# Performance work log

Measured on AMD Instinct MI355X. Metric: run time of the kernel, lower is better.

The kernel has to match this reference:

```python
import jax, jax.numpy as jnp
import numpy as np

N, D, H = 4096, 1024, 16
GAMMA = 1.0


def setup_inputs() -> dict:
    key = jax.random.key(0)
    ks = jax.random.split(key, 10)
    s = 1.0 / np.sqrt(D)
    return {
        "x": jax.random.normal(ks[0], (N, D), jnp.float32),
        "h": jax.random.normal(ks[1], (N,), jnp.float32),
        "Wq": jax.random.normal(ks[2], (D, D), jnp.float32) * s,
        "bq": jax.random.normal(ks[3], (D,), jnp.float32) * s,
        "Wk": jax.random.normal(ks[4], (D, D), jnp.float32) * s,
        "bk": jax.random.normal(ks[5], (D,), jnp.float32) * s,
        "Wv": jax.random.normal(ks[6], (D, D), jnp.float32) * s,
        "bv": jax.random.normal(ks[7], (D,), jnp.float32) * s,
        "Wo": jax.random.normal(ks[8], (D, D), jnp.float32) * s,
        "bo": jax.random.normal(ks[9], (D,), jnp.float32) * s,
    }


def reference(x, h, Wq, bq, Wk, bk, Wv, bv, Wo, bo):
    n, d = x.shape
    d_head = d // H
    # torch Linear: y = x @ W.T + b
    q = (x @ Wq.T + bq).reshape(n, H, d_head)
    k = (x @ Wk.T + bk).reshape(n, H, d_head)
    v = (x @ Wv.T + bv).reshape(n, H, d_head)
    scale = 1.0 / np.sqrt(d_head).astype(np.float32)
    logits = jnp.einsum('nhd,mhd->hnm', q, k) * scale  # (H, n, n)
    logits = logits - (GAMMA * h)[None, None, :]       # per-key additive bias
    attn = jax.nn.softmax(logits, axis=-1)
    out = jnp.einsum('hnm,mhd->nhd', attn, v).reshape(n, d)
    return out @ Wo.T + bo + x
```

## Files before the change

kernel.cpp:

```cpp
#include <hip/hip_runtime.h>
#include <hip/hip_bf16.h>
#include <stdint.h>

#define NTOK 4096
#define DM   1024
#define NH   16
#define DH   64
#define SCL  0.1803368801111129f
#define LOG2E 1.4426950408889634f

typedef __attribute__((ext_vector_type(8)))  short bf16x8;
typedef __attribute__((ext_vector_type(4)))  float f32x4;
typedef __attribute__((ext_vector_type(16))) float f32x16;
typedef __attribute__((ext_vector_type(4)))  unsigned short us4;

__device__ inline unsigned short f2bf(float f) {
  union { float f; unsigned int u; } a;
  a.f = f;
  unsigned int u = a.u;
  u += 0x7fffu + ((u >> 16) & 1u);
  return (unsigned short)(u >> 16);
}

__device__ inline unsigned int cvtpk_bf16(float lo, float hi) {
  unsigned int r;
  asm("v_cvt_pk_bf16_f32 %0, %1, %2" : "=v"(r) : "v"(lo), "v"(hi));
  return r;
}

__device__ inline void gload_lds16(const void* gsrc, void* ldst) {
  __builtin_amdgcn_global_load_lds(
      (const __attribute__((address_space(1))) void*)(uintptr_t)gsrc,
      (__attribute__((address_space(3))) void*)(unsigned int)(uintptr_t)ldst,
      16, 0, 0);
}

__global__ void cvt_fused(const float* __restrict__ x,
                          const float* __restrict__ Wq,
                          const float* __restrict__ Wk,
                          const float* __restrict__ Wv,
                          const float* __restrict__ Wo,
                          const float* __restrict__ h,
                          unsigned short* __restrict__ xb,
                          unsigned short* __restrict__ wqkvb,
                          unsigned short* __restrict__ wob,
                          float* __restrict__ hperm) {
  const int b = blockIdx.x;
  if (b >= 8192) {
    int i = (b - 8192) * 256 + threadIdx.x;
    int r  = i & 15;
    int hh = (i >> 4) & 1;
    int t  = i >> 5;
    int key = t * 32 + (r & 3) + 8 * (r >> 2) + 4 * hh;
    hperm[i] = -LOG2E * h[key];
    return;
  }
  int i = b * 256 + threadIdx.x;
  const float* src; unsigned short* dst; int off;
  if (i < 1048576)      { src = x;  dst = xb;                 off = i; }
  else if (i < 1310720) { src = Wq; dst = wqkvb;              off = i - 1048576; }
  else if (i < 1572864) { src = Wk; dst = wqkvb + DM * DM;    off = i - 1310720; }
  else if (i < 1835008) { src = Wv; dst = wqkvb + 2 * DM * DM; off = i - 1572864; }
  else                  { src = Wo; dst = wob;                off = i - 1835008; }
  float4 v = ((const float4*)src)[off];
  us4 o;
  o[0] = f2bf(v.x); o[1] = f2bf(v.y); o[2] = f2bf(v.z); o[3] = f2bf(v.w);
  ((us4*)dst)[off] = o;
}

__global__ __launch_bounds__(256)
void gemm_qkv(const unsigned short* __restrict__ A,
              const unsigned short* __restrict__ B,
              const float* __restrict__ bq, const float* __restrict__ bk,
              const float* __restrict__ bv,
              unsigned short* __restrict__ Qb, unsigned short* __restrict__ Kb,
              unsigned short* __restrict__ Vt)
{
  const int tid  = threadIdx.x;
  const int wid  = tid >> 6;
  const int lane = tid & 63;
  const int bn = blockIdx.x * 128;
  const int bm = blockIdx.y * 128;
  const int wr = wid >> 1;
  const int wc = wid & 1;

  __shared__ __align__(16) unsigned short As[128 * 32];
  __shared__ __align__(16) unsigned short Bs[128 * 32];

  f32x4 acc[4][4];
#pragma unroll
  for (int i = 0; i < 4; i++)
#pragma unroll
    for (int j = 0; j < 4; j++) acc[i][j] = f32x4{0.f, 0.f, 0.f, 0.f};

  const int fr = lane & 15;
  const int fk = (lane >> 4) * 8;
  const int srow = lane >> 2;
  const int scol = (lane & 3) * 8;

  for (int k0 = 0; k0 < DM; k0 += 32) {
#pragma unroll
    for (int c = 0; c < 2; ++c) {
      const int chunk = wid * 2 + c;
      gload_lds16(A + (size_t)(bm + chunk * 16 + srow) * DM + k0 + scol,
                  &As[chunk * 512]);
      gload_lds16(B + (size_t)(bn + chunk * 16 + srow) * DM + k0 + scol,
                  &Bs[chunk * 512]);
    }
    __syncthreads();
    bf16x8 af[4], bfr[4];
#pragma unroll
    for (int i = 0; i < 4; i++)
      af[i] = *(const bf16x8*)&As[(wr * 64 + i * 16 + fr) * 32 + fk];
#pragma unroll
    for (int j = 0; j < 4; j++)
      bfr[j] = *(const bf16x8*)&Bs[(wc * 64 + j * 16 + fr) * 32 + fk];
#pragma unroll
    for (int i = 0; i < 4; i++)
#pragma unroll
      for (int j = 0; j < 4; j++)
        acc[i][j] = __builtin_amdgcn_mfma_f32_16x16x32_bf16(af[i], bfr[j],
                                                            acc[i][j], 0, 0, 0);
    __syncthreads();
  }

  const int fq = lane >> 4;
  const int region = bn >> 10;
  const float* bias = (region == 0) ? bq : (region == 1) ? bk : bv;
  const float qscale = (region == 0) ? SCL : 1.0f;
  unsigned short* outp = (region == 0) ? Qb : Kb;
#pragma unroll
  for (int j = 0; j < 4; j++) {
    const int col = bn + wc * 64 + j * 16 + fr;
    const int cl  = col & 1023;
    const float bvx = bias[cl];
#pragma unroll
    for (int i = 0; i < 4; i++) {
      const int row0 = bm + wr * 64 + i * 16 + fq * 4;
      if (region < 2) {
#pragma unroll
        for (int r = 0; r < 4; r++)
          outp[(size_t)(row0 + r) * DM + cl] = f2bf((acc[i][j][r] + bvx) * qscale);
      } else {
        us4 pk;
#pragma unroll
        for (int r = 0; r < 4; r++) pk[r] = f2bf(acc[i][j][r] + bvx);
        *(us4*)&Vt[(size_t)cl * NTOK + row0] = pk;
      }
    }
  }
}

__global__ __launch_bounds__(256)
void gemm_out(const unsigned short* __restrict__ A,
              const unsigned short* __restrict__ B,
              const float* __restrict__ bias,
              const float* __restrict__ resid,
              float* __restrict__ Cf)
{
  const int tid  = threadIdx.x;
  const int wid  = tid >> 6;
  const int lane = tid & 63;
  const int bn = blockIdx.x * 128;
  const int bm = blockIdx.y * 128;
  const int wr = wid >> 1;
  const int wc = wid & 1;

  __shared__ __align__(16) unsigned short As[128 * 32];
  __shared__ __align__(16) unsigned short Bs[128 * 32];

  f32x4 acc[4][4];
#pragma unroll
  for (int i = 0; i < 4; i++)
#pragma unroll
    for (int j = 0; j < 4; j++) acc[i][j] = f32x4{0.f, 0.f, 0.f, 0.f};

  const int fr = lane & 15;
  const int fk = (lane >> 4) * 8;
  const int srow = lane >> 2;
  const int scol = (lane & 3) * 8;

  for (int k0 = 0; k0 < DM; k0 += 32) {
#pragma unroll
    for (int c = 0; c < 2; ++c) {
      const int chunk = wid * 2 + c;
      gload_lds16(A + (size_t)(bm + chunk * 16 + srow) * DM + k0 + scol,
                  &As[chunk * 512]);
      gload_lds16(B + (size_t)(bn + chunk * 16 + srow) * DM + k0 + scol,
                  &Bs[chunk * 512]);
    }
    __syncthreads();
    bf16x8 af[4], bfr[4];
#pragma unroll
    for (int i = 0; i < 4; i++)
      af[i] = *(const bf16x8*)&As[(wr * 64 + i * 16 + fr) * 32 + fk];
#pragma unroll
    for (int j = 0; j < 4; j++)
      bfr[j] = *(const bf16x8*)&Bs[(wc * 64 + j * 16 + fr) * 32 + fk];
#pragma unroll
    for (int i = 0; i < 4; i++)
#pragma unroll
      for (int j = 0; j < 4; j++)
        acc[i][j] = __builtin_amdgcn_mfma_f32_16x16x32_bf16(af[i], bfr[j],
                                                            acc[i][j], 0, 0, 0);
    __syncthreads();
  }

  const int fq = lane >> 4;
#pragma unroll
  for (int j = 0; j < 4; j++) {
    const int col = bn + wc * 64 + j * 16 + fr;
    const float bvx = bias[col];
#pragma unroll
    for (int i = 0; i < 4; i++) {
      const int row0 = bm + wr * 64 + i * 16 + fq * 4;
#pragma unroll
      for (int r = 0; r < 4; r++) {
        const size_t idx = (size_t)(row0 + r) * DM + col;
        Cf[idx] = acc[i][j][r] + bvx + resid[idx];
      }
    }
  }
}

#define MFMA32(a, b, c) __builtin_amdgcn_mfma_f32_32x32x16_bf16(a, b, c, 0, 0, 0)

__global__ __launch_bounds__(512)
void attn_kernel(const unsigned short* __restrict__ Q,
                 const unsigned short* __restrict__ K,
                 const unsigned short* __restrict__ Vt,
                 const float* __restrict__ hperm,
                 unsigned short* __restrict__ O)
{
  const int wgid = (blockIdx.x & 7) * 64 + (blockIdx.x >> 3);
  const int head = wgid >> 5;
  const int qblk = wgid & 31;
  const int tid  = threadIdx.x;
  const int wid  = tid >> 6;
  const int grp  = wid >> 2;
  const int w4   = wid & 3;
  const int lane = tid & 63;
  const int c31  = lane & 31;
  const int hi   = lane >> 5;
  const int qwb  = qblk * 128 + w4 * 32;
  const int k0g  = grp * 2048;

  __shared__ __align__(16) char lds_raw[32768];
  char* kbase = lds_raw + grp * 16384;
  char* vbase = kbase + 8192;

  const int srow = w4 * 4 + (lane >> 4);
  const int ssl  = lane & 15;
  const int kq   = ssl ^ srow;
  const int kkey = srow + 16 * (kq >> 3);
  const unsigned short* kg =
      K + (size_t)(k0g + kkey) * DM + head * DH + (kq & 7) * 8;
  const int vd = (kq >> 2) * 16 + srow;
  const unsigned short* vg =
      Vt + (size_t)(head * DH + vd) * NTOK + k0g + (kq & 3) * 8;

  const int fr15 = c31 & 15;
  const int fkh  = c31 >> 4;
  int koffB[4], voffB[2][2];
#pragma unroll
  for (int f = 0; f < 4; f++)
    koffB[f] = fr15 * 256 + (((fkh * 8 + f * 2 + hi) ^ fr15) << 4);
#pragma unroll
  for (int db = 0; db < 2; db++)
#pragma unroll
    for (int ko = 0; ko < 2; ko++)
      voffB[db][ko] =
          fr15 * 256 + ((((db * 2 + fkh) * 4 + ko * 2 + hi) ^ fr15) << 4);

  const unsigned short* qp = Q + (size_t)(qwb + c31) * DM + head * DH + hi * 8;
  const bf16x8 qf0 = *(const bf16x8*)(qp);
  const bf16x8 qf1 = *(const bf16x8*)(qp + 16);
  const bf16x8 qf2 = *(const bf16x8*)(qp + 32);
  const bf16x8 qf3 = *(const bf16x8*)(qp + 48);

  f32x16 o0, o1;
#pragma unroll
  for (int i = 0; i < 16; i++) { o0[i] = 0.f; o1[i] = 0.f; }
  float l = 0.f;

  gload_lds16(kg, kbase + w4 * 1024);
  gload_lds16(vg, vbase + w4 * 1024);
  __syncthreads();

  int cur = 0;
  const int NT = 2048 / 32;
  for (int t = 0; t < NT; ++t) {
    if (t + 1 < NT) {
      gload_lds16(kg + (size_t)(t + 1) * 32 * DM,
                  kbase + (cur ^ 1) * 4096 + w4 * 1024);
      gload_lds16(vg + (t + 1) * 32,
                  vbase + (cur ^ 1) * 4096 + w4 * 1024);
    }

    const float* hp = hperm + k0g + t * 32 + hi * 16;
    const float4 b0 = *(const float4*)(hp + 0);
    const float4 b1 = *(const float4*)(hp + 4);
    const float4 b2 = *(const float4*)(hp + 8);
    const float4 b3 = *(const float4*)(hp + 12);

    const char* Kb = kbase + cur * 4096;
    const char* Vb = vbase + cur * 4096;
    const bf16x8 kf0 = *(const bf16x8*)(Kb + koffB[0]);
    const bf16x8 kf1 = *(const bf16x8*)(Kb + koffB[1]);
    const bf16x8 kf2 = *(const bf16x8*)(Kb + koffB[2]);
    const bf16x8 kf3 = *(const bf16x8*)(Kb + koffB[3]);

    f32x16 s;
    s[0]  = b0.x; s[1]  = b0.y; s[2]  = b0.z; s[3]  = b0.w;
    s[4]  = b1.x; s[5]  = b1.y; s[6]  = b1.z; s[7]  = b1.w;
    s[8]  = b2.x; s[9]  = b2.y; s[10] = b2.z; s[11] = b2.w;
    s[12] = b3.x; s[13] = b3.y; s[14] = b3.z; s[15] = b3.w;

    s = MFMA32(kf0, qf0, s);
    s = MFMA32(kf1, qf1, s);
    s = MFMA32(kf2, qf2, s);
    s = MFMA32(kf3, qf3, s);

    const bf16x8 v00 = *(const bf16x8*)(Vb + voffB[0][0]);
    const bf16x8 v01 = *(const bf16x8*)(Vb + voffB[0][1]);
    const bf16x8 v10 = *(const bf16x8*)(Vb + voffB[1][0]);
    const bf16x8 v11 = *(const bf16x8*)(Vb + voffB[1][1]);

    float ps[16];
#pragma unroll
    for (int r = 0; r < 16; r++) ps[r] = __builtin_amdgcn_exp2f(s[r]);
    l += (((ps[0] + ps[1]) + (ps[2] + ps[3])) +
          ((ps[4] + ps[5]) + (ps[6] + ps[7]))) +
         (((ps[8] + ps[9]) + (ps[10] + ps[11])) +
          ((ps[12] + ps[13]) + (ps[14] + ps[15])));

    unsigned int X1 = cvtpk_bf16(ps[0],  ps[1]);
    unsigned int X2 = cvtpk_bf16(ps[2],  ps[3]);
    unsigned int Y1 = cvtpk_bf16(ps[4],  ps[5]);
    unsigned int Y2 = cvtpk_bf16(ps[6],  ps[7]);
    asm("v_permlane32_swap_b32 %0, %1" : "+v"(X1), "+v"(Y1));
    asm("v_permlane32_swap_b32 %0, %1" : "+v"(X2), "+v"(Y2));
    unsigned int X3 = cvtpk_bf16(ps[8],  ps[9]);
    unsigned int X4 = cvtpk_bf16(ps[10], ps[11]);
    unsigned int Y3 = cvtpk_bf16(ps[12], ps[13]);
    unsigned int Y4 = cvtpk_bf16(ps[14], ps[15]);
    asm("v_permlane32_swap_b32 %0, %1" : "+v"(X3), "+v"(Y3));
    asm("v_permlane32_swap_b32 %0, %1" : "+v"(X4), "+v"(Y4));

    union { unsigned int u[4]; bf16x8 v; } P0, P1;
    P0.u[0] = X1; P0.u[1] = X2; P0.u[2] = Y1; P0.u[3] = Y2;
    P1.u[0] = X3; P1.u[1] = X4; P1.u[2] = Y3; P1.u[3] = Y4;

    o0 = MFMA32(v00, P0.v, o0);
    o0 = MFMA32(v01, P1.v, o0);
    o1 = MFMA32(v10, P0.v, o1);
    o1 = MFMA32(v11, P1.v, o1);

    __syncthreads();
    cur ^= 1;
  }

  l += __shfl_xor(l, 32, 64);

  float* mo = (float*)lds_raw;
  float* mL = (float*)(lds_raw + 17408);
  float* row = &mo[(w4 * 64 + lane) * 17];
#pragma unroll
  for (int half = 0; half < 2; half++) {
    __syncthreads();
    if (grp == 1) {
      const f32x16& hA = half ? o1 : o0;
#pragma unroll
      for (int i = 0; i < 16; i++) row[i] = hA[i];
      if (half == 0 && hi == 0) mL[w4 * 32 + c31] = l;
    }
    __syncthreads();
    if (grp == 0) {
      f32x16& hA = half ? o1 : o0;
#pragma unroll
      for (int i = 0; i < 16; i++) hA[i] += row[i];
      if (half == 0) l += mL[w4 * 32 + c31];
    }
  }

  if (grp == 0) {
    const float inv = 1.0f / l;
    unsigned short* ob = O + (size_t)(qwb + c31) * DM + head * DH;
#pragma unroll
    for (int g = 0; g < 4; g++) {
      us4 pk;
      pk[0] = f2bf(o0[4 * g + 0] * inv); pk[1] = f2bf(o0[4 * g + 1] * inv);
      pk[2] = f2bf(o0[4 * g + 2] * inv); pk[3] = f2bf(o0[4 * g + 3] * inv);
      *(us4*)(ob + 8 * g + 4 * hi) = pk;
      pk[0] = f2bf(o1[4 * g + 0] * inv); pk[1] = f2bf(o1[4 * g + 1] * inv);
      pk[2] = f2bf(o1[4 * g + 2] * inv); pk[3] = f2bf(o1[4 * g + 3] * inv);
      *(us4*)(ob + 32 + 8 * g + 4 * hi) = pk;
    }
  }
}

extern "C" void kernel_launch(void* const* d_in, const int* in_sizes, int n_in,
                              void* d_out, int out_size, void* d_ws, size_t ws_size,
                              hipStream_t stream) {
  const float* x  = (const float*)d_in[0];
  const float* h  = (const float*)d_in[1];
  const float* Wq = (const float*)d_in[2];
  const float* bq = (const float*)d_in[3];
  const float* Wk = (const float*)d_in[4];
  const float* bk = (const float*)d_in[5];
  const float* Wv = (const float*)d_in[6];
  const float* bv = (const float*)d_in[7];
  const float* Wo = (const float*)d_in[8];
  const float* bo = (const float*)d_in[9];
  float* out = (float*)d_out;

  char* ws = (char*)d_ws;
  const size_t MB = 1 << 20;
  unsigned short* xb    = (unsigned short*)(ws + 0 * MB);
  unsigned short* wqkvb = (unsigned short*)(ws + 8 * MB);
  unsigned short* wob   = (unsigned short*)(ws + 14 * MB);
  unsigned short* Qb    = (unsigned short*)(ws + 16 * MB);
  unsigned short* Kb    = (unsigned short*)(ws + 24 * MB);
  unsigned short* Vtb   = (unsigned short*)(ws + 32 * MB);
  unsigned short* AOb   = (unsigned short*)(ws + 40 * MB);
  float*          hperm = (float*)(ws + 48 * MB);

  cvt_fused<<<8208, 256, 0, stream>>>(x, Wq, Wk, Wv, Wo, h,
                                      xb, wqkvb, wob, hperm);

  gemm_qkv<<<dim3(24, 32), 256, 0, stream>>>(xb, wqkvb, bq, bk, bv, Qb, Kb, Vtb);

  attn_kernel<<<dim3(512), 512, 0, stream>>>(Qb, Kb, Vtb, hperm, AOb);

  gemm_out<<<dim3(DM / 128, NTOK / 128), 256, 0, stream>>>(AOb, wob, bo, x, out);
}
```

Baseline: 169.6 us.

## Triple-buffer K/V LDS tiles with vmcnt-based waits and MFMA priority hints

Moves the attention inner loop from double to triple buffering of K/V tiles in LDS. Each iteration prefetches two tiles ahead and waits with s_waitcnt vmcnt(2) before a raw s_barrier instead of a full __syncthreads. This is meant to hide global-to-LDS latency and avoid draining all outstanding loads every iteration. It also raises wave priority around the MFMA groups, and costs 50% more LDS per block, which may reduce occupancy.

```diff
diff --git a/kernel.cpp b/kernel.cpp
--- a/kernel.cpp
+++ b/kernel.cpp
@@ -245,9 +245,9 @@
   const int qwb  = qblk * 128 + w4 * 32;
   const int k0g  = grp * 2048;
 
-  __shared__ __align__(16) char lds_raw[32768];
-  char* kbase = lds_raw + grp * 16384;
-  char* vbase = kbase + 8192;
+  __shared__ __align__(16) char lds_raw[49152];
+  char* kbase = lds_raw + grp * 24576;
+  char* vbase = kbase + 12288;
 
   const int srow = w4 * 4 + (lane >> 4);
   const int ssl  = lane & 15;
@@ -258,6 +258,7 @@
   const int vd = (kq >> 2) * 16 + srow;
   const unsigned short* vg =
       Vt + (size_t)(head * DH + vd) * NTOK + k0g + (kq & 3) * 8;
+  const int sdst = w4 * 1024;
 
   const int fr15 = c31 & 15;
   const int fkh  = c31 >> 4;
@@ -283,25 +284,26 @@
   for (int i = 0; i < 16; i++) { o0[i] = 0.f; o1[i] = 0.f; }
   float l = 0.f;
 
-  gload_lds16(kg, kbase + w4 * 1024);
-  gload_lds16(vg, vbase + w4 * 1024);
-  __syncthreads();
-
-  int cur = 0;
+  gload_lds16(kg, kbase + sdst);
+  gload_lds16(vg, vbase + sdst);
+  gload_lds16(kg + (size_t)32 * DM, kbase + 4096 + sdst);
+  gload_lds16(vg + 32, vbase + 4096 + sdst);
+  asm volatile("s_waitcnt vmcnt(2)");
+  __builtin_amdgcn_sched_barrier(0);
+  __builtin_amdgcn_s_barrier();
+
+  int cur = 0, nxt = 1, stg = 2;
   const int NT = 2048 / 32;
   for (int t = 0; t < NT; ++t) {
-    if (t + 1 < NT) {
-      gload_lds16(kg + (size_t)(t + 1) * 32 * DM,
-                  kbase + (cur ^ 1) * 4096 + w4 * 1024);
-      gload_lds16(vg + (t + 1) * 32,
-                  vbase + (cur ^ 1) * 4096 + w4 * 1024);
-    }
-
     const float* hp = hperm + k0g + t * 32 + hi * 16;
     const float4 b0 = *(const float4*)(hp + 0);
     const float4 b1 = *(const float4*)(hp + 4);
     const float4 b2 = *(const float4*)(hp + 8);
     const float4 b3 = *(const float4*)(hp + 12);
+
+    const int ts = (t + 2 < NT) ? (t + 2) : (NT - 1);
+    gload_lds16(kg + (size_t)ts * 32 * DM, kbase + stg * 4096 + sdst);
+    gload_lds16(vg + ts * 32, vbase + stg * 4096 + sdst);
 
     const char* Kb = kbase + cur * 4096;
     const char* Vb = vbase + cur * 4096;
@@ -316,10 +318,12 @@
     s[8]  = b2.x; s[9]  = b2.y; s[10] = b2.z; s[11] = b2.w;
     s[12] = b3.x; s[13] = b3.y; s[14] = b3.z; s[15] = b3.w;
 
+    __builtin_amdgcn_s_setprio(1);
     s = MFMA32(kf0, qf0, s);
     s = MFMA32(kf1, qf1, s);
     s = MFMA32(kf2, qf2, s);
     s = MFMA32(kf3, qf3, s);
+    __builtin_amdgcn_s_setprio(0);
 
     const bf16x8 v00 = *(const bf16x8*)(Vb + voffB[0][0]);
     const bf16x8 v01 = *(const bf16x8*)(Vb + voffB[0][1]);
@@ -351,13 +355,18 @@
     P0.u[0] = X1; P0.u[1] = X2; P0.u[2] = Y1; P0.u[3] = Y2;
     P1.u[0] = X3; P1.u[1] = X4; P1.u[2] = Y3; P1.u[3] = Y4;
 
+    __builtin_amdgcn_s_setprio(1);
     o0 = MFMA32(v00, P0.v, o0);
     o0 = MFMA32(v01, P1.v, o0);
     o1 = MFMA32(v10, P0.v, o1);
     o1 = MFMA32(v11, P1.v, o1);
-
-    __syncthreads();
-    cur ^= 1;
+    __builtin_amdgcn_s_setprio(0);
+
+    asm volatile("s_waitcnt vmcnt(2)");
+    __builtin_amdgcn_sched_barrier(0);
+    __builtin_amdgcn_s_barrier();
+
+    const int tmp = cur; cur = nxt; nxt = stg; stg = tmp;
   }
 
   l += __shfl_xor(l, 32, 64);
```

Result: slower. 173.5 us (+2.3%).

## Shrink output GEMM tile to 128x64 and compute softmax row sums via MFMA

Applied to the files above, without the earlier changes.

The output projection GEMM now uses 128x64 tiles with each wave owning 32 rows, which doubles the grid to 512 blocks for better CU occupancy, at the cost of more operand reloads. In the attention kernel, the scalar VALU accumulation of the softmax denominator is replaced by an extra pair of MFMAs against a ones-vector, moving 15 adds per iteration onto the matrix unit. In exchange it adds MFMA work and a third accumulator's registers, and the sum is taken from bf16-rounded probabilities.

```diff
diff --git a/kernel.cpp b/kernel.cpp
--- a/kernel.cpp
+++ b/kernel.cpp
@@ -161,17 +161,15 @@
   const int tid  = threadIdx.x;
   const int wid  = tid >> 6;
   const int lane = tid & 63;
-  const int bn = blockIdx.x * 128;
+  const int bn = blockIdx.x * 64;
   const int bm = blockIdx.y * 128;
-  const int wr = wid >> 1;
-  const int wc = wid & 1;
 
   __shared__ __align__(16) unsigned short As[128 * 32];
-  __shared__ __align__(16) unsigned short Bs[128 * 32];
-
-  f32x4 acc[4][4];
-#pragma unroll
-  for (int i = 0; i < 4; i++)
+  __shared__ __align__(16) unsigned short Bs[64 * 32];
+
+  f32x4 acc[2][4];
+#pragma unroll
+  for (int i = 0; i < 2; i++)
 #pragma unroll
     for (int j = 0; j < 4; j++) acc[i][j] = f32x4{0.f, 0.f, 0.f, 0.f};
 
@@ -182,23 +180,26 @@
 
   for (int k0 = 0; k0 < DM; k0 += 32) {
 #pragma unroll
-    for (int c = 0; c < 2; ++c) {
-      const int chunk = wid * 2 + c;
-      gload_lds16(A + (size_t)(bm + chunk * 16 + srow) * DM + k0 + scol,
-                  &As[chunk * 512]);
-      gload_lds16(B + (size_t)(bn + chunk * 16 + srow) * DM + k0 + scol,
-                  &Bs[chunk * 512]);
-    }
-    __syncthreads();
-    bf16x8 af[4], bfr[4];
-#pragma unroll
-    for (int i = 0; i < 4; i++)
-      af[i] = *(const bf16x8*)&As[(wr * 64 + i * 16 + fr) * 32 + fk];
+    for (int c = 0; c < 3; ++c) {
+      const int chunk = wid * 3 + c;
+      if (chunk < 8) {
+        gload_lds16(A + (size_t)(bm + chunk * 16 + srow) * DM + k0 + scol,
+                    &As[chunk * 512]);
+      } else {
+        gload_lds16(B + (size_t)(bn + (chunk - 8) * 16 + srow) * DM + k0 + scol,
+                    &Bs[(chunk - 8) * 512]);
+      }
+    }
+    __syncthreads();
+    bf16x8 af[2], bfr[4];
+#pragma unroll
+    for (int i = 0; i < 2; i++)
+      af[i] = *(const bf16x8*)&As[(wid * 32 + i * 16 + fr) * 32 + fk];
 #pragma unroll
     for (int j = 0; j < 4; j++)
-      bfr[j] = *(const bf16x8*)&Bs[(wc * 64 + j * 16 + fr) * 32 + fk];
-#pragma unroll
-    for (int i = 0; i < 4; i++)
+      bfr[j] = *(const bf16x8*)&Bs[(j * 16 + fr) * 32 + fk];
+#pragma unroll
+    for (int i = 0; i < 2; i++)
 #pragma unroll
       for (int j = 0; j < 4; j++)
         acc[i][j] = __builtin_amdgcn_mfma_f32_16x16x32_bf16(af[i], bfr[j],
@@ -209,11 +210,11 @@
   const int fq = lane >> 4;
 #pragma unroll
   for (int j = 0; j < 4; j++) {
-    const int col = bn + wc * 64 + j * 16 + fr;
+    const int col = bn + j * 16 + fr;
     const float bvx = bias[col];
 #pragma unroll
-    for (int i = 0; i < 4; i++) {
-      const int row0 = bm + wr * 64 + i * 16 + fq * 4;
+    for (int i = 0; i < 2; i++) {
+      const int row0 = bm + wid * 32 + i * 16 + fq * 4;
 #pragma unroll
       for (int r = 0; r < 4; r++) {
         const size_t idx = (size_t)(row0 + r) * DM + col;
@@ -278,10 +279,13 @@
   const bf16x8 qf2 = *(const bf16x8*)(qp + 32);
   const bf16x8 qf3 = *(const bf16x8*)(qp + 48);
 
-  f32x16 o0, o1;
-#pragma unroll
-  for (int i = 0; i < 16; i++) { o0[i] = 0.f; o1[i] = 0.f; }
-  float l = 0.f;
+  const unsigned int onesw = (c31 == 0) ? 0x3F803F80u : 0u;
+  union { unsigned int u[4]; bf16x8 v; } ONE;
+  ONE.u[0] = onesw; ONE.u[1] = onesw; ONE.u[2] = onesw; ONE.u[3] = onesw;
+
+  f32x16 o0, o1, o2;
+#pragma unroll
+  for (int i = 0; i < 16; i++) { o0[i] = 0.f; o1[i] = 0.f; o2[i] = 0.f; }
 
   gload_lds16(kg, kbase + w4 * 1024);
   gload_lds16(vg, vbase + w4 * 1024);
@@ -329,10 +333,6 @@
     float ps[16];
 #pragma unroll
     for (int r = 0; r < 16; r++) ps[r] = __builtin_amdgcn_exp2f(s[r]);
-    l += (((ps[0] + ps[1]) + (ps[2] + ps[3])) +
-          ((ps[4] + ps[5]) + (ps[6] + ps[7]))) +
-         (((ps[8] + ps[9]) + (ps[10] + ps[11])) +
-          ((ps[12] + ps[13]) + (ps[14] + ps[15])));
 
     unsigned int X1 = cvtpk_bf16(ps[0],  ps[1]);
     unsigned int X2 = cvtpk_bf16(ps[2],  ps[3]);
@@ -355,11 +355,14 @@
     o0 = MFMA32(v01, P1.v, o0);
     o1 = MFMA32(v10, P0.v, o1);
     o1 = MFMA32(v11, P1.v, o1);
+    o2 = MFMA32(ONE.v, P0.v, o2);
+    o2 = MFMA32(ONE.v, P1.v, o2);
 
     __syncthreads();
     cur ^= 1;
   }
 
+  float l = o2[0];
   l += __shfl_xor(l, 32, 64);
 
   float* mo = (float*)lds_raw;
@@ -432,5 +435,5 @@
 
   attn_kernel<<<dim3(512), 512, 0, stream>>>(Qb, Kb, Vtb, hperm, AOb);
 
-  gemm_out<<<dim3(DM / 128, NTOK / 128), 256, 0, stream>>>(AOb, wob, bo, x, out);
-}
+  gemm_out<<<dim3(DM / 64, NTOK / 128), 256, 0, stream>>>(AOb, wob, bo, x, out);
+}
```

After: 170.4 us. About the same (+0.5%).
